# Kernel tuning notes

Hardware: AMD Instinct MI355X
Metric: run time of the kernel (lower is better)

## Reference

```python
import jax, jax.numpy as jnp
import numpy as np

NS, NR, NT = 16, 128, 4096   # shots, receivers, time samples
NP = 100                      # quantile knots (p = linspace(0,1,100) in source)
DT = 1e-3                     # time step
FILT = 5                      # uniform_filter size for q_deriv smoothing
HP = 1.0 / (NP - 1)           # uniform p-knot spacing


def cum_trap(y, dx):
    # cumulative trapezoid along last dim, length-preserving (leading 0)
    c = jnp.cumsum(0.5 * (y[..., 1:] + y[..., :-1]), axis=-1) * dx
    return jnp.concatenate([jnp.zeros_like(y[..., :1]), c], axis=-1)


def trap(y, dx):
    return dx * (jnp.sum(y, axis=-1) - 0.5 * (y[..., 0] + y[..., -1]))


def renorm(f, dx):
    # |f| normalized to a PDF via trapezoidal rule
    a = jnp.abs(f)
    return a / trap(a, dx)[..., None]


def natural_cubic_coeffs(h, y):
    # natural cubic spline on a uniform grid; y: [..., n] -> coeffs [..., 4, n-1]
    n = y.shape[-1]
    rhs = 6.0 * (y[..., 2:] - 2.0 * y[..., 1:-1] + y[..., :-2]) / (h * h)
    A = (4.0 * jnp.eye(n - 2) + jnp.eye(n - 2, k=1) + jnp.eye(n - 2, k=-1)).astype(y.dtype)
    M_int = jnp.linalg.solve(A, rhs[..., None])[..., 0]
    M = jnp.pad(M_int, [(0, 0)] * (y.ndim - 1) + [(1, 1)])  # natural BCs: M0 = Mn-1 = 0
    a = y[..., :-1]
    b = (y[..., 1:] - y[..., :-1]) / h - h * (2.0 * M[..., :-1] + M[..., 1:]) / 6.0
    c = M[..., :-1] / 2.0
    d = (M[..., 1:] - M[..., :-1]) / (6.0 * h)
    return jnp.stack([a, b, c, d], axis=-2)


def spline_eval(coeffs, h, x, deriv=False):
    # per-trace cubic spline eval: coeffs [..., 4, n-1], x [..., m] in [0, 1]
    a, b, c, d = coeffs[..., 0, :], coeffs[..., 1, :], coeffs[..., 2, :], coeffs[..., 3, :]
    n1 = a.shape[-1]
    xi = jnp.clip(x, 0.0, n1 * h)
    idx = jnp.clip((xi / h).astype(jnp.int32), 0, n1 - 1)
    dxv = xi - idx.astype(x.dtype) * h
    g = lambda z: jnp.take_along_axis(z, idx, axis=-1)
    ai, bi, ci, di = g(a), g(b), g(c), g(d)
    if deriv:
        return bi + dxv * (2.0 * ci + 3.0 * di * dxv)
    return ai + dxv * (bi + dxv * (ci + di * dxv))


def uniform_filter1d(x, size=FILT):
    r = size // 2
    xp = jnp.pad(x, [(0, 0)] * (x.ndim - 1) + [(r, r)], mode='symmetric')
    return sum(xp[..., i:i + x.shape[-1]] for i in range(size)) / size


def build_splines(obs_data, t):
    # cts_quantile: CDF of renormalized obs, inverted at p grid, then cubic spline
    dt = t[1] - t[0]
    p = jnp.linspace(0.0, 1.0, NP, dtype=obs_data.dtype)
    F_obs = cum_trap(renorm(obs_data, dt), dt)                    # [NS,NR,NT]
    flat = F_obs.reshape(-1, F_obs.shape[-1])
    Q = jax.vmap(lambda Fi: jnp.interp(p, Fi, t))(flat)           # quantile knots
    Q = Q.reshape(*F_obs.shape[:-1], NP)
    qc = natural_cubic_coeffs(HP, Q)                              # quantile spline
    d1 = spline_eval(qc, HP, jnp.broadcast_to(p, Q.shape), deriv=True)
    d1 = uniform_filter1d(d1)                                     # filter_func
    qdc = natural_cubic_coeffs(HP, d1)                            # q_deriv spline
    return qc, qdc


def setup_inputs() -> dict:
    key = jax.random.key(0)
    k1, k2 = jax.random.split(key)
    f = jax.random.normal(k1, (NS, NR, NT), dtype=jnp.float32)
    obs_data = jax.random.normal(k2, (NS, NR, NT), dtype=jnp.float32)
    t = jnp.arange(NT, dtype=jnp.float32) * DT
    return {"f": f, "obs_data": obs_data, "t": t}


def reference(f, obs_data, t):
    dt = t[1] - t[0]
    qc, _ = build_splines(obs_data, t)
    f_tilde = renorm(f, dt)
    F = cum_trap(f_tilde, dt)                    # per-trace CDF, values in [0,1]
    off_diag = spline_eval(qc, HP, F)            # Q_obs(F(t)) spline gather
    diff = t - off_diag
    integrated = trap(diff * diff * f_tilde, dt)
    return integrated.sum()
```

## Files before the change

### kernel.cpp

```cpp
#include <hip/hip_runtime.h>

#define NT 4096
#define NPP 100
#define NROWS 2048
#define BLK 256
#define EPT 16
#define NM 98
#define DTIME 0.001f
#define HF (1.0f / 99.0f)

__device__ __constant__ float GW[13] = {
    0.288675135f,    -0.077350269f,   0.020725943f,   -0.0055534374f,
    0.0014880647f,   -0.00039874667f, 0.00010684152f, -2.8626968e-05f,
    7.6707195e-06f,  -2.0554928e-06f, 5.5072549e-07f, -1.4756630e-07f,
    3.9539424e-08f};

__device__ __forceinline__ int swz(int k) { return k + (k >> 4); }

__global__ __launch_bounds__(BLK) void wass_row_kernel(
    const float* __restrict__ f, const float* __restrict__ obs,
    float* __restrict__ rowOut) {
  const int row  = blockIdx.x;
  const int tid  = threadIdx.x;
  const int lane = tid & 63;
  const int wid  = tid >> 6;

  __shared__ float sF[NT + NT / 16];
  __shared__ float sQ[NPP];
  __shared__ float sWo[4], sWf[4], sWoOff[4], sWfOff[4];
  __shared__ float sTotO, sTotF, sY0o, sYlo, sY0f, sYlf;
  float* sRhs = sF;
  float* sM   = sF + 128;
  float4* sCo = (float4*)(sF + 256);

  float yo[EPT], yf[EPT];
  {
    const float4* op = (const float4*)(obs + (size_t)row * NT);
    const float4* fp = (const float4*)(f + (size_t)row * NT);
    float4 vo[4], vf[4];
#pragma unroll
    for (int q = 0; q < 4; ++q) vo[q] = op[tid * 4 + q];
#pragma unroll
    for (int q = 0; q < 4; ++q) vf[q] = fp[tid * 4 + q];
#pragma unroll
    for (int q = 0; q < 4; ++q) {
      yo[4*q+0] = fabsf(vo[q].x); yo[4*q+1] = fabsf(vo[q].y);
      yo[4*q+2] = fabsf(vo[q].z); yo[4*q+3] = fabsf(vo[q].w);
      yf[4*q+0] = fabsf(vf[q].x); yf[4*q+1] = fabsf(vf[q].y);
      yf[4*q+2] = fabsf(vf[q].z); yf[4*q+3] = fabsf(vf[q].w);
    }
  }

  float so = 0.f, sf = 0.f;
#pragma unroll
  for (int j = 0; j < EPT; ++j) { so += yo[j]; sf += yf[j]; }
  float vo = so, vf = sf;
#pragma unroll
  for (int off = 1; off < 64; off <<= 1) {
    float no = __shfl_up(vo, off, 64);
    float nf = __shfl_up(vf, off, 64);
    if (lane >= off) { vo += no; vf += nf; }
  }
  if (lane == 63) { sWo[wid] = vo; sWf[wid] = vf; }
  if (tid == 0)       { sY0o = yo[0];       sY0f = yf[0]; }
  if (tid == BLK - 1) { sYlo = yo[EPT - 1]; sYlf = yf[EPT - 1]; }
  __syncthreads();
  if (tid == 0) {
    float a = 0.f, b = 0.f;
#pragma unroll
    for (int w = 0; w < 4; ++w) {
      sWoOff[w] = a; a += sWo[w];
      sWfOff[w] = b; b += sWf[w];
    }
    sTotO = a; sTotF = b;
  }
  __syncthreads();

  const float exO0 = (vo - so) + sWoOff[wid];
  const float exF0 = (vf - sf) + sWfOff[wid];
  const float y0f  = sY0f;
  const float TrF  = sTotF - 0.5f * (sY0f + sYlf);
  const float invTF = 1.0f / TrF;

  {
    const float invT = 1.0f / (sTotO - 0.5f * (sY0o + sYlo));
    const float hInv = 0.5f * invT;
    const float c0   = sY0o * hInv;
    float ex = exO0;
    int b17 = tid * 17;
#pragma unroll
    for (int j = 0; j < EPT; ++j) {
      sF[b17 + j] = fmaf(ex, invT, fmaf(yo[j], hInv, -c0));
      ex += yo[j];
    }
  }
  __syncthreads();

  if (tid < NPP) {
    float x = (float)((double)tid * (1.0 / 99.0));
    int lo = 0, hi = NT;
#pragma unroll
    for (int it = 0; it < 12; ++it) {
      int mid = (lo + hi) >> 1;
      float v = sF[swz(mid)];
      if (v > x) hi = mid; else lo = mid + 1;
    }
    int i = lo;
    if (i < 1) i = 1;
    if (i > NT - 1) i = NT - 1;
    float Fj = sF[swz(i - 1)], Fi = sF[swz(i)];
    float dxv = Fi - Fj;
    float tj = (float)(i - 1) * DTIME;
    float qv = (dxv == 0.0f) ? (float)i * DTIME
                             : fmaf((x - Fj) / dxv, DTIME, tj);
    sQ[tid] = qv;
  }
  __syncthreads();

  if (tid < NM) {
    sRhs[tid] = (6.0f * 99.0f * 99.0f) *
                (sQ[tid + 2] - 2.0f * sQ[tid + 1] + sQ[tid]);
  }
  __syncthreads();

  if (tid < NM) {
    float m = 0.f;
#pragma unroll
    for (int d = -12; d <= 12; ++d) {
      int j = tid + d;
      bool neg = (j < 0), pos = (j > NM - 1);
      int jr = neg ? (-2 - j) : (pos ? (2 * NM - j) : j);
      jr = jr < 0 ? 0 : (jr > NM - 1 ? NM - 1 : jr);
      bool z = (j == -1) || (j == NM);
      float v = sRhs[jr];
      v = (neg || pos) ? -v : v;
      v = z ? 0.f : v;
      m = fmaf(GW[d < 0 ? -d : d], v, m);
    }
    sM[tid + 1] = m;
  }
  if (tid == NM) { sM[0] = 0.f; sM[NPP - 1] = 0.f; }
  __syncthreads();

  if (tid < NPP - 1) {
    float yi = sQ[tid], yi1 = sQ[tid + 1];
    float Mi = sM[tid], Mi1 = sM[tid + 1];
    float4 co;
    co.x = yi;
    co.y = (yi1 - yi) * 99.0f - HF * (2.0f * Mi + Mi1) * (1.0f / 6.0f);
    co.z = 0.5f * Mi;
    co.w = (Mi1 - Mi) * (99.0f / 6.0f);
    sCo[tid] = co;
  }
  __syncthreads();

  float acc = 0.f;
  {
    const float hInv = 0.5f * invTF;
    const float c0   = y0f * hInv;
    float ex = exF0;
    const float tBase = (float)(tid * EPT) * DTIME;
#pragma unroll
    for (int j = 0; j < EPT; ++j) {
      int k = tid * EPT + j;
      float yv = yf[j];
      float Fk = fmaf(ex, invTF, fmaf(yv, hInv, -c0));
      ex += yv;
      float xi = fminf(fmaxf(Fk, 0.f), 1.f);
      int idx = (int)(xi * 99.0f);
      if (idx > NPP - 2) idx = NPP - 2;
      float dxv = fmaf(-(float)idx, HF, xi);
      float4 co = sCo[idx];
      float val = fmaf(dxv, fmaf(dxv, fmaf(dxv, co.w, co.z), co.y), co.x);
      float tk = fmaf((float)j, DTIME, tBase);
      float diff = tk - val;
      float w = (k == 0 || k == NT - 1) ? 0.5f : 1.0f;
      acc = fmaf(w * diff, diff * yv, acc);
    }
  }

#pragma unroll
  for (int off = 32; off > 0; off >>= 1) acc += __shfl_down(acc, off, 64);
  if (lane == 0) sWo[wid] = acc;
  __syncthreads();
  if (tid == 0) {
    rowOut[row] = (sWo[0] + sWo[1] + sWo[2] + sWo[3]) * invTF;
  }
}

__global__ __launch_bounds__(256) void wass_reduce_kernel(
    const float* __restrict__ rowOut, float* __restrict__ out) {
  __shared__ double sW[4];
  int tid = threadIdx.x;
  int lane = tid & 63, wid = tid >> 6;
  double acc = 0.0;
  for (int i = tid; i < NROWS; i += 256) acc += (double)rowOut[i];
#pragma unroll
  for (int off = 32; off > 0; off >>= 1) acc += __shfl_down(acc, off, 64);
  if (lane == 0) sW[wid] = acc;
  __syncthreads();
  if (tid == 0) out[0] = (float)(sW[0] + sW[1] + sW[2] + sW[3]);
}

extern "C" void kernel_launch(void* const* d_in, const int* in_sizes, int n_in,
                              void* d_out, int out_size, void* d_ws, size_t ws_size,
                              hipStream_t stream) {
  (void)in_sizes; (void)n_in; (void)out_size; (void)ws_size;
  const float* f   = (const float*)d_in[0];
  const float* obs = (const float*)d_in[1];
  float* rowOut = (float*)d_ws;

  wass_row_kernel<<<NROWS, BLK, 0, stream>>>(f, obs, rowOut);
  wass_reduce_kernel<<<1, 256, 0, stream>>>(rowOut, (float*)d_out);
}
```

Before: 99.95 us.

## Fuse final reduction via atomicAdd and drop trapezoid endpoint weights

Replaces the second reduction kernel with a per-block atomicAdd into the output, zeroed first by a memset. This removes the second kernel launch and the workspace round trip. It also drops the 0.5 trapezoid weighting on the first and last samples of each row, which changes the result slightly and removes a compare from the inner loop. The float atomic makes the summation order nondeterministic and loses the double-precision accumulation.

```diff
diff --git a/kernel.cpp b/kernel.cpp
--- a/kernel.cpp
+++ b/kernel.cpp
@@ -19,7 +19,7 @@
 
 __global__ __launch_bounds__(BLK) void wass_row_kernel(
     const float* __restrict__ f, const float* __restrict__ obs,
-    float* __restrict__ rowOut) {
+    float* __restrict__ out) {
   const int row  = blockIdx.x;
   const int tid  = threadIdx.x;
   const int lane = tid & 63;
@@ -162,7 +162,6 @@
     const float tBase = (float)(tid * EPT) * DTIME;
 #pragma unroll
     for (int j = 0; j < EPT; ++j) {
-      int k = tid * EPT + j;
       float yv = yf[j];
       float Fk = fmaf(ex, invTF, fmaf(yv, hInv, -c0));
       ex += yv;
@@ -172,10 +171,8 @@
       float dxv = fmaf(-(float)idx, HF, xi);
       float4 co = sCo[idx];
       float val = fmaf(dxv, fmaf(dxv, fmaf(dxv, co.w, co.z), co.y), co.x);
-      float tk = fmaf((float)j, DTIME, tBase);
-      float diff = tk - val;
-      float w = (k == 0 || k == NT - 1) ? 0.5f : 1.0f;
-      acc = fmaf(w * diff, diff * yv, acc);
+      float diff = fmaf((float)j, DTIME, tBase) - val;
+      acc = fmaf(diff * diff, yv, acc);
     }
   }
 
@@ -184,32 +181,17 @@
   if (lane == 0) sWo[wid] = acc;
   __syncthreads();
   if (tid == 0) {
-    rowOut[row] = (sWo[0] + sWo[1] + sWo[2] + sWo[3]) * invTF;
+    atomicAdd(out, (sWo[0] + sWo[1] + sWo[2] + sWo[3]) * invTF);
   }
-}
-
-__global__ __launch_bounds__(256) void wass_reduce_kernel(
-    const float* __restrict__ rowOut, float* __restrict__ out) {
-  __shared__ double sW[4];
-  int tid = threadIdx.x;
-  int lane = tid & 63, wid = tid >> 6;
-  double acc = 0.0;
-  for (int i = tid; i < NROWS; i += 256) acc += (double)rowOut[i];
-#pragma unroll
-  for (int off = 32; off > 0; off >>= 1) acc += __shfl_down(acc, off, 64);
-  if (lane == 0) sW[wid] = acc;
-  __syncthreads();
-  if (tid == 0) out[0] = (float)(sW[0] + sW[1] + sW[2] + sW[3]);
 }
 
 extern "C" void kernel_launch(void* const* d_in, const int* in_sizes, int n_in,
                               void* d_out, int out_size, void* d_ws, size_t ws_size,
                               hipStream_t stream) {
-  (void)in_sizes; (void)n_in; (void)out_size; (void)ws_size;
+  (void)in_sizes; (void)n_in; (void)out_size; (void)d_ws; (void)ws_size;
   const float* f   = (const float*)d_in[0];
   const float* obs = (const float*)d_in[1];
-  float* rowOut = (float*)d_ws;
 
-  wass_row_kernel<<<NROWS, BLK, 0, stream>>>(f, obs, rowOut);
-  wass_reduce_kernel<<<1, 256, 0, stream>>>(rowOut, (float*)d_out);
+  hipMemsetAsync(d_out, 0, sizeof(float), stream);
+  wass_row_kernel<<<NROWS, BLK, 0, stream>>>(f, obs, (float*)d_out);
 }
```

New measurement: 120.9 us. 20.9% more time.

## Compute quantile knots by per-thread crossing scatter instead of binary search

Applied to the files above, without the earlier changes.

Builds the quantile knots by having each thread scan its own 16 CDF values in registers and write the knots whose levels fall inside its segment, seeded with the previous thread's last value. This removes the 4096-entry shared CDF array, one barrier and the 12-step dependent binary search run by only 100 threads. Shared memory per block drops sharply, which may allow more resident blocks. It also drops the 0.5 endpoint trapezoid weights, relying on the integrand being near zero at both ends; this adds a small numerical risk.

```diff
diff --git a/kernel.cpp b/kernel.cpp
--- a/kernel.cpp
+++ b/kernel.cpp
@@ -15,8 +15,6 @@
     7.6707195e-06f,  -2.0554928e-06f, 5.5072549e-07f, -1.4756630e-07f,
     3.9539424e-08f};
 
-__device__ __forceinline__ int swz(int k) { return k + (k >> 4); }
-
 __global__ __launch_bounds__(BLK) void wass_row_kernel(
     const float* __restrict__ f, const float* __restrict__ obs,
     float* __restrict__ rowOut) {
@@ -25,13 +23,13 @@
   const int lane = tid & 63;
   const int wid  = tid >> 6;
 
-  __shared__ float sF[NT + NT / 16];
-  __shared__ float sQ[NPP];
-  __shared__ float sWo[4], sWf[4], sWoOff[4], sWfOff[4];
-  __shared__ float sTotO, sTotF, sY0o, sYlo, sY0f, sYlf;
-  float* sRhs = sF;
-  float* sM   = sF + 128;
-  float4* sCo = (float4*)(sF + 256);
+  __shared__ float  sQ[NPP];
+  __shared__ float  sM[NPP];
+  __shared__ float  sRhs[NM];
+  __shared__ float4 sCo[NPP - 1];
+  __shared__ float  sFlast[BLK];
+  __shared__ float  sWo[4], sWf[4], sWoOff[4], sWfOff[4];
+  __shared__ float  sTotO, sTotF, sY0o, sYlo, sY0f, sYlf;
 
   float yo[EPT], yf[EPT];
   {
@@ -87,33 +85,44 @@
     const float hInv = 0.5f * invT;
     const float c0   = sY0o * hInv;
     float ex = exO0;
-    int b17 = tid * 17;
 #pragma unroll
     for (int j = 0; j < EPT; ++j) {
-      sF[b17 + j] = fmaf(ex, invT, fmaf(yo[j], hInv, -c0));
-      ex += yo[j];
-    }
-  }
-  __syncthreads();
-
-  if (tid < NPP) {
-    float x = (float)((double)tid * (1.0 / 99.0));
-    int lo = 0, hi = NT;
-#pragma unroll
-    for (int it = 0; it < 12; ++it) {
-      int mid = (lo + hi) >> 1;
-      float v = sF[swz(mid)];
-      if (v > x) hi = mid; else lo = mid + 1;
-    }
-    int i = lo;
-    if (i < 1) i = 1;
-    if (i > NT - 1) i = NT - 1;
-    float Fj = sF[swz(i - 1)], Fi = sF[swz(i)];
-    float dxv = Fi - Fj;
-    float tj = (float)(i - 1) * DTIME;
-    float qv = (dxv == 0.0f) ? (float)i * DTIME
-                             : fmaf((x - Fj) / dxv, DTIME, tj);
-    sQ[tid] = qv;
+      float yv = yo[j];
+      yo[j] = fmaf(ex, invT, fmaf(yv, hInv, -c0));
+      ex += yv;
+    }
+    sFlast[tid] = yo[EPT - 1];
+  }
+  if (tid == 0) sQ[0] = 0.0f;
+  __syncthreads();
+
+  {
+    float a = (tid == 0) ? 0.0f : sFlast[tid - 1];
+    int kprev = (int)floorf(a * 99.0f);
+    if (kprev < 0) kprev = 0;
+    const int base = tid * EPT;
+#pragma unroll
+    for (int j = 0; j < EPT; ++j) {
+      float b = yo[j];
+      int k0 = base + j;
+      int kb = (int)floorf(b * 99.0f);
+      if (kb > 99) kb = 99;
+      if (k0 == NT - 1) kb = 99;
+      if (kb > kprev) {
+        float denom = b - a;
+        float tPrev = (float)(k0 - 1) * DTIME;
+        bool ok = denom > 0.f;
+        float rd = ok ? 1.0f / denom : 0.0f;
+        for (int k = kprev + 1; k <= kb; ++k) {
+          float pk = (float)k * HF;
+          float r = ok ? (pk - a) * rd : 1.0f;
+          r = fminf(r, 1.0f);
+          sQ[k] = fmaf(r, DTIME, tPrev);
+        }
+        kprev = kb;
+      }
+      a = b;
+    }
   }
   __syncthreads();
 
@@ -162,7 +171,6 @@
     const float tBase = (float)(tid * EPT) * DTIME;
 #pragma unroll
     for (int j = 0; j < EPT; ++j) {
-      int k = tid * EPT + j;
       float yv = yf[j];
       float Fk = fmaf(ex, invTF, fmaf(yv, hInv, -c0));
       ex += yv;
@@ -172,10 +180,8 @@
       float dxv = fmaf(-(float)idx, HF, xi);
       float4 co = sCo[idx];
       float val = fmaf(dxv, fmaf(dxv, fmaf(dxv, co.w, co.z), co.y), co.x);
-      float tk = fmaf((float)j, DTIME, tBase);
-      float diff = tk - val;
-      float w = (k == 0 || k == NT - 1) ? 0.5f : 1.0f;
-      acc = fmaf(w * diff, diff * yv, acc);
+      float diff = fmaf((float)j, DTIME, tBase) - val;
+      acc = fmaf(diff * diff, yv, acc);
     }
   }
 
```

Result: slower. 105.3 us (+5.4%).
